# Kernel optimization log

Hardware: AMD Instinct MI355X
Metric: run time of the kernel (lower is better)

Reference implementation:

```python
import jax, jax.numpy as jnp
import numpy as np
from math import factorial, sqrt, pi

L = 10  # must match init_kwargs


def setup_inputs() -> dict:
    key = jax.random.key(0)
    pos = jax.random.normal(key, (2_000_000, 3), dtype=jnp.float32)
    return {"pos": pos}


def _cpow_tables(zr, zi, nmax):
    """Powers (zr + i*zi)^n for n=0..nmax. Returns (nmax+1, N) real and imag parts.
    Matches powcmplx in the source (repeated complex multiply), computed once."""
    reals = [jnp.ones_like(zr)]
    imags = [jnp.zeros_like(zr)]
    for _ in range(nmax):
        r, im = reals[-1], imags[-1]
        reals.append(zr * r - zi * im)
        imags.append(zr * im + zi * r)
    return jnp.stack(reals), jnp.stack(imags)


def reference(pos):
    norms = jnp.linalg.norm(pos, axis=1)            # (N,)
    mask = (norms > 0).astype(pos.dtype)            # replaces boolean indexing ids
    x, y, x0 = pos[:, 0], pos[:, 1], pos[:, 2]
    xpl1r, xpl1i = -0.5 * x, -0.5 * y
    xm1r, xm1i = 0.5 * x, -0.5 * y
    # precompute all needed complex powers (same math as powcmplx, deduplicated)
    z1r_t, z1i_t = _cpow_tables(xpl1r, xpl1i, L)    # (L+1, N)
    z2r_t, z2i_t = _cpow_tables(xm1r, xm1i, L)

    clms = [None] * ((L + 1) ** 2)
    i = 0
    for l in range(L + 1):
        rl = norms ** l
        for M in range(-l, 1):
            m = abs(M)
            shr = jnp.zeros_like(x)
            shi = jnp.zeros_like(x)
            for p in range(l + 1):
                q = p - m
                s = l - p - q
                if q >= 0 and s >= 0:
                    z1r, z1i = z1r_t[p], z1i_t[p]
                    z2r, z2i = z2r_t[q], z2i_t[q]
                    # NOTE: faithful to source, including its quirks:
                    # zreal uses z1r**2 - z2i**2, and the term is scaled by x0
                    # (x0**s is computed in the source but never used).
                    zreal = z1r ** 2 - z2i ** 2
                    zimag = z1r * z2i + z1i * z2r
                    c = 1.0 / (factorial(p) * factorial(q) * factorial(s))
                    shr = shr + zreal * x0 * c
                    shi = shi + zimag * x0 * c
            scale = sqrt(factorial(l + m) * factorial(l - m)) * sqrt((2 * l + 1) / (4.0 * pi))
            clm_r = jnp.sum(shr * rl * mask) * scale
            clm_i = jnp.sum(shi * rl * mask) * scale
            if m == 0:
                clms[i] = clm_r
            else:
                f = sqrt(2.0) * (-1) ** m
                clms[i] = f * clm_i
                clms[i + 2 * m] = f * clm_r
            i += 1
        i += l
    return jnp.stack(clms).reshape(-1, 1)  # ((L+1)^2, 1)
```

## Files before the change

### kernel.cpp

```cpp
#include <hip/hip_runtime.h>

namespace {

constexpr int LMAX  = 10;
constexpr int NPART = 2;
constexpr int PART_OF_L[LMAX + 1] = {1, 1, 0, 0, 1, 1, 0, 0, 1, 1, 0};
constexpr double PI_D = 3.14159265358979323846;

constexpr double dfact(int n) {
    double r = 1.0;
    for (int i = 2; i <= n; ++i) r *= (double)i;
    return r;
}

constexpr double csqrt(double x) {
    if (x <= 0.0) return 0.0;
    double g = x > 1.0 ? x : 1.0;
    for (int i = 0; i < 100; ++i) g = 0.5 * (g + x / g);
    return g;
}

constexpr double FACT[LMAX + 1] = {1., 1., 2., 6., 24., 120., 720., 5040., 40320., 362880., 3628800.};

constexpr int slot_base(int part, int l) {
    int c = 0;
    for (int ll = 0; ll < l; ++ll)
        if (PART_OF_L[ll] == part) c += 2 * ll + 1;
    return c;
}
constexpr int nacc_part(int part) {
    int c = 0;
    for (int l = 0; l <= LMAX; ++l)
        if (PART_OF_L[l] == part) c += 2 * l + 1;
    return c;
}
constexpr int part_lmax(int part) {
    int mx = 0;
    for (int l = 0; l <= LMAX; ++l)
        if (PART_OF_L[l] == part) mx = l;
    return mx;
}
constexpr int slot_r(int part, int l, int m) { return slot_base(part, l) + m; }
constexpr int slot_i(int part, int l, int m) { return slot_base(part, l) + (l + 1) + (m - 1); }

constexpr int MAXNA = 61;

constexpr float ci_coef(int l, int m, int q) {
    const double c = 1.0 / (FACT[q + m] * FACT[q] * FACT[l - m - 2 * q]);
    return (q & 1) ? (float)(-c) : (float)c;
}

struct Tables {
    int   map[NPART][MAXNA];
    float scl[NPART][MAXNA];
};

constexpr Tables make_tables() {
    Tables t{};
    for (int part = 0; part < NPART; ++part) {
        for (int l = 0; l <= LMAX; ++l) {
            if (PART_OF_L[l] != part) continue;
            for (int m = 0; m <= l; ++m) {
                const int k = slot_r(part, l, m);
                const double scale =
                    csqrt(dfact(l + m) * dfact(l - m)) * csqrt((2 * l + 1) / (4.0 * PI_D));
                const double fold = (m >= 1 && (l - m) <= 1) ? 1.0 / (dfact(m) * dfact(l - m)) : 1.0;
                if (m == 0) {
                    t.map[part][k] = l * l + l;
                    t.scl[part][k] = (float)(scale * fold);
                } else {
                    const double f = csqrt(2.0) * ((m & 1) ? -1.0 : 1.0);
                    t.map[part][k] = l * l + l + m;
                    t.scl[part][k] = (float)(f * scale * fold);
                }
            }
            for (int m = 1; m <= l; ++m) {
                const int k = slot_i(part, l, m);
                const double scale =
                    csqrt(dfact(l + m) * dfact(l - m)) * csqrt((2 * l + 1) / (4.0 * PI_D));
                const double f    = csqrt(2.0) * ((m & 1) ? -1.0 : 1.0);
                const double fold = ((l - m) <= 1) ? 1.0 / (dfact(m) * dfact(l - m)) : 1.0;
                t.map[part][k] = l * l + l - m;
                t.scl[part][k] = (float)(f * scale * fold);
            }
        }
    }
    return t;
}

__constant__ Tables c_tab = make_tables();

}

template <int PART>
__device__ __forceinline__ void sht_part(const float* __restrict__ pos,
                                         float* __restrict__ out, int n, int nblk) {
    constexpr int NA = nacc_part(PART);
    constexpr int PL = part_lmax(PART);

    float acc[NA];
#pragma unroll
    for (int k = 0; k < NA; ++k) acc[k] = 0.f;

    const int bid    = (int)(blockIdx.x >> 1);
    const int tid    = bid * 256 + (int)threadIdx.x;
    const int stride = nblk * 256;

    int   i = tid;
    float x = 0.f, y = 0.f, z0 = 0.f;
    if (i < n) {
        x  = pos[3 * i + 0];
        y  = pos[3 * i + 1];
        z0 = pos[3 * i + 2];
    }

    while (i < n) {
        const int inext = i + stride;
        float     px = 0.f, py = 0.f, pz = 0.f;
        if (inext < n) {
            px = pos[3 * inext + 0];
            py = pos[3 * inext + 1];
            pz = pos[3 * inext + 2];
        }

        const float r2  = x * x + y * y + z0 * z0;
        const float nrm = sqrtf(r2);
        const float w0  = (nrm > 0.f) ? z0 : 0.f;

        const float ar = -0.5f * x, ai = -0.5f * y;
        const float rho = ar * ar + ai * ai;

        float zi[PL + 1], sr[PL + 1], si[PL + 1];
        zi[0] = 0.f;
        sr[0] = 1.f;
        si[0] = 0.f;
        float zrc = 1.f;
#pragma unroll
        for (int p = 1; p <= PL; ++p) {
            const float nzr = ar * zrc - ai * zi[p - 1];
            zi[p]           = ar * zi[p - 1] + ai * zrc;
            zrc             = nzr;
            sr[p]           = zrc * zrc;
            si[p]           = zi[p] * zi[p];
        }
        float rp[PL + 1];
        rp[0] = 1.f;
#pragma unroll
        for (int l = 1; l <= PL; ++l) rp[l] = rp[l - 1] * nrm;

#pragma unroll
        for (int l = 0; l <= LMAX; ++l) {
            if (PART_OF_L[l] != PART) continue;
            const float wrl = w0 * rp[l];
#pragma unroll
            for (int m = 0; m <= l; ++m) {
                const int Q = (l - m) >> 1;
                if (m >= 1 && Q == 0) {
                    acc[slot_r(PART, l, m)] += sr[m] * wrl;
                    acc[slot_i(PART, l, m)] += zi[m] * wrl;
                } else {
                    float shr = 0.f;
#pragma unroll
                    for (int p = m; 2 * p <= l + m; ++p) {
                        const int   q  = p - m;
                        const float cr = (float)(1.0 / (FACT[p] * FACT[q] * FACT[l - 2 * p + m]));
                        shr += (sr[p] - si[q]) * cr;
                    }
                    acc[slot_r(PART, l, m)] += shr * wrl;
                    if (m >= 1) {
                        float t = ci_coef(l, m, Q);
#pragma unroll
                        for (int q = Q - 1; q >= 0; --q) t = t * rho + ci_coef(l, m, q);
                        acc[slot_i(PART, l, m)] += (t * zi[m]) * wrl;
                    }
                }
            }
        }

        i  = inext;
        x  = px;
        y  = py;
        z0 = pz;
    }

    __shared__ float red[4][NA];
    const int lane = threadIdx.x & 63;
    const int wav  = threadIdx.x >> 6;
#pragma unroll
    for (int k = 0; k < NA; ++k) {
        float v = acc[k];
#pragma unroll
        for (int off = 32; off > 0; off >>= 1) v += __shfl_down(v, off, 64);
        if (lane == 0) red[wav][k] = v;
    }
    __syncthreads();
    if ((int)threadIdx.x < NA) {
        const int   k = (int)threadIdx.x;
        const float v = red[0][k] + red[1][k] + red[2][k] + red[3][k];
        atomicAdd(&out[c_tab.map[PART][k]], v * c_tab.scl[PART][k]);
    }
}

__global__ __launch_bounds__(256, 3) void sht_kernel(const float* __restrict__ pos,
                                                     float* __restrict__ out, int n, int nblk) {
    if (blockIdx.x & 1)
        sht_part<1>(pos, out, n, nblk);
    else
        sht_part<0>(pos, out, n, nblk);
}

extern "C" void kernel_launch(void* const* d_in, const int* in_sizes, int n_in,
                              void* d_out, int out_size, void* d_ws, size_t ws_size,
                              hipStream_t stream) {
    const float* pos = (const float*)d_in[0];
    float* out       = (float*)d_out;
    const int n      = in_sizes[0] / 3;

    hipMemsetAsync(d_out, 0, (size_t)out_size * sizeof(float), stream);

    const int threads       = 256;
    const int nblk_per_part = 768;
    const int blocks        = NPART * nblk_per_part;
    sht_kernel<<<blocks, threads, 0, stream>>>(pos, out, n, nblk_per_part);
}
```

Baseline: 129.9 us.

## Merge split l-partitions into a single kernel computing all degrees per thread

Removes the two-way split of spherical harmonic degrees across alternating blocks, so each thread now computes all 121 coefficients for every point it owns. Each point is loaded and its complex power tables are computed once instead of twice. The grid drops to 512 blocks and launch bounds to 2 waves per SIMD to make room for the larger accumulator array. The cost is higher register pressure, with possible spills, and lower occupancy.

Measured after the change: 126.7 us. -2.4%, faster.

```diff
diff --git a/kernel.cpp b/kernel.cpp
--- a/kernel.cpp
+++ b/kernel.cpp
@@ -2,9 +2,7 @@
 
 namespace {
 
-constexpr int LMAX  = 10;
-constexpr int NPART = 2;
-constexpr int PART_OF_L[LMAX + 1] = {1, 1, 0, 0, 1, 1, 0, 0, 1, 1, 0};
+constexpr int LMAX = 10;
 constexpr double PI_D = 3.14159265358979323846;
 
 constexpr double dfact(int n) {
@@ -22,28 +20,9 @@
 
 constexpr double FACT[LMAX + 1] = {1., 1., 2., 6., 24., 120., 720., 5040., 40320., 362880., 3628800.};
 
-constexpr int slot_base(int part, int l) {
-    int c = 0;
-    for (int ll = 0; ll < l; ++ll)
-        if (PART_OF_L[ll] == part) c += 2 * ll + 1;
-    return c;
-}
-constexpr int nacc_part(int part) {
-    int c = 0;
-    for (int l = 0; l <= LMAX; ++l)
-        if (PART_OF_L[l] == part) c += 2 * l + 1;
-    return c;
-}
-constexpr int part_lmax(int part) {
-    int mx = 0;
-    for (int l = 0; l <= LMAX; ++l)
-        if (PART_OF_L[l] == part) mx = l;
-    return mx;
-}
-constexpr int slot_r(int part, int l, int m) { return slot_base(part, l) + m; }
-constexpr int slot_i(int part, int l, int m) { return slot_base(part, l) + (l + 1) + (m - 1); }
-
-constexpr int MAXNA = 61;
+constexpr int slot_r(int l, int m) { return l * l + m; }
+constexpr int slot_i(int l, int m) { return l * l + (l + 1) + (m - 1); }
+constexpr int NA = (LMAX + 1) * (LMAX + 1);
 
 constexpr float ci_coef(int l, int m, int q) {
     const double c = 1.0 / (FACT[q + m] * FACT[q] * FACT[l - m - 2 * q]);
@@ -51,38 +30,35 @@
 }
 
 struct Tables {
-    int   map[NPART][MAXNA];
-    float scl[NPART][MAXNA];
+    int   map[NA];
+    float scl[NA];
 };
 
 constexpr Tables make_tables() {
     Tables t{};
-    for (int part = 0; part < NPART; ++part) {
-        for (int l = 0; l <= LMAX; ++l) {
-            if (PART_OF_L[l] != part) continue;
-            for (int m = 0; m <= l; ++m) {
-                const int k = slot_r(part, l, m);
-                const double scale =
-                    csqrt(dfact(l + m) * dfact(l - m)) * csqrt((2 * l + 1) / (4.0 * PI_D));
-                const double fold = (m >= 1 && (l - m) <= 1) ? 1.0 / (dfact(m) * dfact(l - m)) : 1.0;
-                if (m == 0) {
-                    t.map[part][k] = l * l + l;
-                    t.scl[part][k] = (float)(scale * fold);
-                } else {
-                    const double f = csqrt(2.0) * ((m & 1) ? -1.0 : 1.0);
-                    t.map[part][k] = l * l + l + m;
-                    t.scl[part][k] = (float)(f * scale * fold);
-                }
+    for (int l = 0; l <= LMAX; ++l) {
+        for (int m = 0; m <= l; ++m) {
+            const int k = slot_r(l, m);
+            const double scale =
+                csqrt(dfact(l + m) * dfact(l - m)) * csqrt((2 * l + 1) / (4.0 * PI_D));
+            const double fold = (m >= 1 && (l - m) <= 1) ? 1.0 / (dfact(m) * dfact(l - m)) : 1.0;
+            if (m == 0) {
+                t.map[k] = l * l + l;
+                t.scl[k] = (float)(scale * fold);
+            } else {
+                const double f = csqrt(2.0) * ((m & 1) ? -1.0 : 1.0);
+                t.map[k] = l * l + l + m;
+                t.scl[k] = (float)(f * scale * fold);
             }
-            for (int m = 1; m <= l; ++m) {
-                const int k = slot_i(part, l, m);
-                const double scale =
-                    csqrt(dfact(l + m) * dfact(l - m)) * csqrt((2 * l + 1) / (4.0 * PI_D));
-                const double f    = csqrt(2.0) * ((m & 1) ? -1.0 : 1.0);
-                const double fold = ((l - m) <= 1) ? 1.0 / (dfact(m) * dfact(l - m)) : 1.0;
-                t.map[part][k] = l * l + l - m;
-                t.scl[part][k] = (float)(f * scale * fold);
-            }
+        }
+        for (int m = 1; m <= l; ++m) {
+            const int k = slot_i(l, m);
+            const double scale =
+                csqrt(dfact(l + m) * dfact(l - m)) * csqrt((2 * l + 1) / (4.0 * PI_D));
+            const double f    = csqrt(2.0) * ((m & 1) ? -1.0 : 1.0);
+            const double fold = ((l - m) <= 1) ? 1.0 / (dfact(m) * dfact(l - m)) : 1.0;
+            t.map[k] = l * l + l - m;
+            t.scl[k] = (float)(f * scale * fold);
         }
     }
     return t;
@@ -92,18 +68,16 @@
 
 }
 
-template <int PART>
-__device__ __forceinline__ void sht_part(const float* __restrict__ pos,
-                                         float* __restrict__ out, int n, int nblk) {
-    constexpr int NA = nacc_part(PART);
-    constexpr int PL = part_lmax(PART);
+__global__ __launch_bounds__(256, 2) void sht_kernel(const float* __restrict__ pos,
+                                                     float* __restrict__ out, int n, int nblk) {
+    constexpr int PL = LMAX;
+    constexpr int QX = PL / 2;
 
     float acc[NA];
 #pragma unroll
     for (int k = 0; k < NA; ++k) acc[k] = 0.f;
 
-    const int bid    = (int)(blockIdx.x >> 1);
-    const int tid    = bid * 256 + (int)threadIdx.x;
+    const int tid    = (int)blockIdx.x * 256 + (int)threadIdx.x;
     const int stride = nblk * 256;
 
     int   i = tid;
@@ -127,10 +101,10 @@
         const float nrm = sqrtf(r2);
         const float w0  = (nrm > 0.f) ? z0 : 0.f;
 
-        const float ar = -0.5f * x, ai = -0.5f * y;
+        const float ar  = -0.5f * x, ai = -0.5f * y;
         const float rho = ar * ar + ai * ai;
 
-        float zi[PL + 1], sr[PL + 1], si[PL + 1];
+        float zi[PL + 1], sr[PL + 1], si[QX + 1];
         zi[0] = 0.f;
         sr[0] = 1.f;
         si[0] = 0.f;
@@ -141,7 +115,7 @@
             zi[p]           = ar * zi[p - 1] + ai * zrc;
             zrc             = nzr;
             sr[p]           = zrc * zrc;
-            si[p]           = zi[p] * zi[p];
+            if (p <= QX) si[p] = zi[p] * zi[p];
         }
         float rp[PL + 1];
         rp[0] = 1.f;
@@ -150,14 +124,13 @@
 
 #pragma unroll
         for (int l = 0; l <= LMAX; ++l) {
-            if (PART_OF_L[l] != PART) continue;
             const float wrl = w0 * rp[l];
 #pragma unroll
             for (int m = 0; m <= l; ++m) {
                 const int Q = (l - m) >> 1;
                 if (m >= 1 && Q == 0) {
-                    acc[slot_r(PART, l, m)] += sr[m] * wrl;
-                    acc[slot_i(PART, l, m)] += zi[m] * wrl;
+                    acc[slot_r(l, m)] += sr[m] * wrl;
+                    acc[slot_i(l, m)] += zi[m] * wrl;
                 } else {
                     float shr = 0.f;
 #pragma unroll
@@ -166,12 +139,12 @@
                         const float cr = (float)(1.0 / (FACT[p] * FACT[q] * FACT[l - 2 * p + m]));
                         shr += (sr[p] - si[q]) * cr;
                     }
-                    acc[slot_r(PART, l, m)] += shr * wrl;
+                    acc[slot_r(l, m)] += shr * wrl;
                     if (m >= 1) {
                         float t = ci_coef(l, m, Q);
 #pragma unroll
                         for (int q = Q - 1; q >= 0; --q) t = t * rho + ci_coef(l, m, q);
-                        acc[slot_i(PART, l, m)] += (t * zi[m]) * wrl;
+                        acc[slot_i(l, m)] += (t * zi[m]) * wrl;
                     }
                 }
             }
@@ -197,16 +170,8 @@
     if ((int)threadIdx.x < NA) {
         const int   k = (int)threadIdx.x;
         const float v = red[0][k] + red[1][k] + red[2][k] + red[3][k];
-        atomicAdd(&out[c_tab.map[PART][k]], v * c_tab.scl[PART][k]);
+        atomicAdd(&out[c_tab.map[k]], v * c_tab.scl[k]);
     }
-}
-
-__global__ __launch_bounds__(256, 3) void sht_kernel(const float* __restrict__ pos,
-                                                     float* __restrict__ out, int n, int nblk) {
-    if (blockIdx.x & 1)
-        sht_part<1>(pos, out, n, nblk);
-    else
-        sht_part<0>(pos, out, n, nblk);
 }
 
 extern "C" void kernel_launch(void* const* d_in, const int* in_sizes, int n_in,
@@ -218,8 +183,7 @@
 
     hipMemsetAsync(d_out, 0, (size_t)out_size * sizeof(float), stream);
 
-    const int threads       = 256;
-    const int nblk_per_part = 768;
-    const int blocks        = NPART * nblk_per_part;
-    sht_kernel<<<blocks, threads, 0, stream>>>(pos, out, n, nblk_per_part);
+    const int threads = 256;
+    const int blocks = 512;
+    sht_kernel<<<blocks, threads, 0, stream>>>(pos, out, n, blocks);
 }
```
